# Kernel optimization log

Hardware: AMD Instinct MI355X
Metric: run time of the kernel (lower is better)

## Reference

```python
import jax, jax.numpy as jnp
import numpy as np

N_ATOMS = 8192
N_FINGERPRINT = 10000
DIM = 64
N_LAYERS = 3
N_MOL = 256


def setup_inputs() -> dict:
    key = jax.random.key(0)
    k1, k2, k3, k4, k5 = jax.random.split(key, 5)
    fingerprints = jax.random.randint(k1, (N_ATOMS,), 0, N_FINGERPRINT)
    adjacencies = jax.random.uniform(k2, (N_ATOMS, N_ATOMS), dtype=jnp.float32)
    segment_ids = jnp.sort(jax.random.randint(k3, (N_ATOMS,), 0, N_MOL))
    embed_table = jax.random.normal(k4, (N_FINGERPRINT, DIM), dtype=jnp.float32) * 0.1
    W = jax.random.normal(k5, (N_LAYERS, DIM, DIM), dtype=jnp.float32) * (1.0 / np.sqrt(DIM))
    b = jnp.zeros((N_LAYERS, DIM), dtype=jnp.float32)
    return {"fingerprints": fingerprints, "adjacencies": adjacencies,
            "segment_ids": segment_ids, "embed_table": embed_table, "W": W, "b": b}


def reference(fingerprints, adjacencies, segment_ids, embed_table, W, b):
    # Embed fingerprint indices -> [N_atoms, dim]
    vectors = embed_table[fingerprints]
    # MPNN layers: h = relu(Linear(v)); v = h + A @ h  (residual message passing)
    for layer in range(N_LAYERS):
        h = jax.nn.relu(jnp.einsum('nd,ed->ne', vectors, W[layer]) + b[layer])
        vectors = h + adjacencies @ h
    # Sum pooling per molecule (torch.split + sum == segment_sum over sorted ids)
    molecular_vectors = jax.ops.segment_sum(vectors, segment_ids, num_segments=N_MOL)
    return molecular_vectors
```

## Files before the change

kernel.cpp:

```cpp
#include <hip/hip_runtime.h>

#define N_ATOMS 8192
#define DIM 64
#define N_MOL 256
#define KS 16
#define KCH (N_ATOMS / KS)
#define BM 64
#define BN 64
#define BK 64
#define NSTEP (KCH / BK)

typedef __attribute__((ext_vector_type(8))) short short8v;
typedef __attribute__((ext_vector_type(4))) float f32x4;
typedef unsigned short ushort_t;

__device__ __forceinline__ ushort_t f2bf(float x) {
    unsigned u = __float_as_uint(x);
    u += 0x7fffu + ((u >> 16) & 1u);
    return (ushort_t)(u >> 16);
}

__device__ __forceinline__ void gload16(const void* gsrc, void* ldst) {
    __builtin_amdgcn_global_load_lds(
        (const __attribute__((address_space(1))) void*)gsrc,
        (__attribute__((address_space(3))) void*)ldst, 16, 0, 0);
}

__device__ __forceinline__ int lower_bound_dev(const int* __restrict__ seg, int val) {
    int lo = 0, hi = N_ATOMS;
    while (lo < hi) {
        int mid = (lo + hi) >> 1;
        if (seg[mid] < val) lo = mid + 1; else hi = mid;
    }
    return lo;
}

__global__ __launch_bounds__(256) void convert_kernel(
        const float* __restrict__ A, ushort_t* __restrict__ Abf) {
    const size_t total = (size_t)N_ATOMS * N_ATOMS;
    const size_t stride = (size_t)gridDim.x * 256 * 8;
    for (size_t i = ((size_t)blockIdx.x * 256 + threadIdx.x) * 8; i < total; i += stride) {
        float4 a0 = *(const float4*)(A + i);
        float4 a1 = *(const float4*)(A + i + 4);
        short8v vv;
        vv[0] = (short)f2bf(a0.x); vv[1] = (short)f2bf(a0.y);
        vv[2] = (short)f2bf(a0.z); vv[3] = (short)f2bf(a0.w);
        vv[4] = (short)f2bf(a1.x); vv[5] = (short)f2bf(a1.y);
        vv[6] = (short)f2bf(a1.z); vv[7] = (short)f2bf(a1.w);
        *(short8v*)(Abf + i) = vv;
    }
}

template <int FIRST>
__global__ __launch_bounds__(256) void fused_linear_kernel(
        const int* __restrict__ fp, const float* __restrict__ table,
        const float* __restrict__ vprev,
        const float* __restrict__ W, const float* __restrict__ b,
        float* __restrict__ vnext, ushort_t* __restrict__ hT) {
    __shared__ float Ws[DIM][DIM + 1];
    __shared__ float vsT[DIM][36];

    const int t = threadIdx.x;
    const int n0 = blockIdx.x * 32;
    for (int i = t; i < DIM * DIM; i += 256) Ws[i >> 6][i & 63] = W[i];
    for (int i = t; i < 32 * DIM; i += 256) {
        const int nl = i >> 6, d = i & 63;
        const size_t n = n0 + nl;
        float val;
        if (FIRST) val = table[(size_t)fp[n] * DIM + d];
        else       val = vprev[n * DIM + d];
        vsT[d][nl] = val;
    }
    __syncthreads();

    const int e = t & 63;
    const int g = t >> 6;
    float acc[8];
    const float be = b[e];
#pragma unroll
    for (int i = 0; i < 8; ++i) acc[i] = be;

    for (int d = 0; d < DIM; ++d) {
        const float w = Ws[e][d];
        const float4* vp = (const float4*)&vsT[d][g * 8];
        float4 x0 = vp[0], x1 = vp[1];
        acc[0] += w * x0.x; acc[1] += w * x0.y; acc[2] += w * x0.z; acc[3] += w * x0.w;
        acc[4] += w * x1.x; acc[5] += w * x1.y; acc[6] += w * x1.z; acc[7] += w * x1.w;
    }

    ushort_t hb[8];
#pragma unroll
    for (int i = 0; i < 8; ++i) {
        float hv = acc[i] > 0.f ? acc[i] : 0.f;
        vnext[(size_t)(n0 + g * 8 + i) * DIM + e] = hv;
        hb[i] = f2bf(hv);
    }
    *(short8v*)(hT + (size_t)e * N_ATOMS + n0 + g * 8) = *(short8v*)&hb[0];
}

__global__ __launch_bounds__(256) void matmul_mfma_kernel(
        const ushort_t* __restrict__ Abf, const ushort_t* __restrict__ hT,
        float* __restrict__ vnext) {
    __shared__ ushort_t Asw[2][BM * BK];
    __shared__ ushort_t Bsw[2][BN * BK];

    const int t  = threadIdx.x;
    const int w  = t >> 6;
    const int l  = t & 63;
    const int lm = l & 15;
    const int lq = l >> 4;
    const int r0 = blockIdx.x * BM;
    const size_t kc0 = (size_t)blockIdx.y * KCH;

    auto stage = [&](int bi, size_t kb) {
#pragma unroll
        for (int q = 0; q < 2; ++q) {
            const int i = q * 256 + t;
            const int r = i >> 3, s = i & 7;
            gload16(Abf + (size_t)(r0 + r) * N_ATOMS + kb + ((s ^ (r & 7)) << 3),
                    &Asw[bi][(q * 256 + w * 64) * 8]);
        }
#pragma unroll
        for (int q = 0; q < 2; ++q) {
            const int i = q * 256 + t;
            const int r = i >> 3, s = i & 7;
            gload16(hT + (size_t)r * N_ATOMS + kb + ((s ^ (r & 7)) << 3),
                    &Bsw[bi][(q * 256 + w * 64) * 8]);
        }
    };

    f32x4 acc[4];
#pragma unroll
    for (int n = 0; n < 4; ++n) acc[n] = (f32x4){0.f, 0.f, 0.f, 0.f};

    stage(0, kc0);

    for (int ks = 0; ks < NSTEP; ++ks) {
        const int bi = ks & 1;
        if (ks + 1 < NSTEP) {
            stage(bi ^ 1, kc0 + (size_t)(ks + 1) * BK);
            asm volatile("s_waitcnt vmcnt(4)" ::: "memory");
        } else {
            asm volatile("s_waitcnt vmcnt(0)" ::: "memory");
        }
        __builtin_amdgcn_s_barrier();
        asm volatile("" ::: "memory");
#pragma unroll
        for (int kki = 0; kki < 2; ++kki) {
            const int sx = ((kki * 4 + lq) ^ (lm & 7)) << 3;
            const int ra = w * 16 + lm;
            short8v a0 = *(const short8v*)&Asw[bi][ra * BK + sx];
            short8v b0 = *(const short8v*)&Bsw[bi][(lm)      * BK + sx];
            short8v b1 = *(const short8v*)&Bsw[bi][(lm + 16) * BK + sx];
            short8v b2 = *(const short8v*)&Bsw[bi][(lm + 32) * BK + sx];
            short8v b3 = *(const short8v*)&Bsw[bi][(lm + 48) * BK + sx];
            acc[0] = __builtin_amdgcn_mfma_f32_16x16x32_bf16(a0, b0, acc[0], 0, 0, 0);
            acc[1] = __builtin_amdgcn_mfma_f32_16x16x32_bf16(a0, b1, acc[1], 0, 0, 0);
            acc[2] = __builtin_amdgcn_mfma_f32_16x16x32_bf16(a0, b2, acc[2], 0, 0, 0);
            acc[3] = __builtin_amdgcn_mfma_f32_16x16x32_bf16(a0, b3, acc[3], 0, 0, 0);
        }
        asm volatile("" ::: "memory");
        __builtin_amdgcn_s_barrier();
        asm volatile("" ::: "memory");
    }

    const int rb = r0 + w * 16 + lq * 4;
#pragma unroll
    for (int j = 0; j < 4; ++j) {
        float* vp = vnext + (size_t)(rb + j) * DIM + lm;
#pragma unroll
        for (int n = 0; n < 4; ++n) atomicAdd(vp + n * 16, acc[n][j]);
    }
}

__global__ __launch_bounds__(256) void segsum_kernel(
        const float* __restrict__ v, const int* __restrict__ seg,
        float* __restrict__ out) {
    __shared__ float sm[4][DIM];
    const int m = blockIdx.x;
    const int d = threadIdx.x & 63;
    const int g = threadIdx.x >> 6;
    const int lo = lower_bound_dev(seg, m);
    const int hi = lower_bound_dev(seg, m + 1);
    float acc = 0.f;
    for (int n = lo + g; n < hi; n += 4) acc += v[(size_t)n * DIM + d];
    sm[g][d] = acc;
    __syncthreads();
    if (g == 0) out[(size_t)m * DIM + d] = sm[0][d] + sm[1][d] + sm[2][d] + sm[3][d];
}

extern "C" void kernel_launch(void* const* d_in, const int* in_sizes, int n_in,
                              void* d_out, int out_size, void* d_ws, size_t ws_size,
                              hipStream_t stream) {
    const int*   fp    = (const int*)d_in[0];
    const float* A     = (const float*)d_in[1];
    const int*   seg   = (const int*)d_in[2];
    const float* table = (const float*)d_in[3];
    const float* W     = (const float*)d_in[4];
    const float* b     = (const float*)d_in[5];
    float* out = (float*)d_out;

    float*    vA  = (float*)d_ws;
    float*    vB  = vA + (size_t)N_ATOMS * DIM;
    ushort_t* hT  = (ushort_t*)(vB + (size_t)N_ATOMS * DIM);
    ushort_t* Abf = hT + (size_t)DIM * N_ATOMS;

    dim3 mmgrid(N_ATOMS / BM, KS);

    convert_kernel<<<2048, 256, 0, stream>>>(A, Abf);
    fused_linear_kernel<1><<<N_ATOMS / 32, 256, 0, stream>>>(
        fp, table, nullptr, W, b, vA, hT);
    matmul_mfma_kernel<<<mmgrid, 256, 0, stream>>>(Abf, hT, vA);
    fused_linear_kernel<0><<<N_ATOMS / 32, 256, 0, stream>>>(
        fp, table, vA, W + DIM * DIM, b + DIM, vB, hT);
    matmul_mfma_kernel<<<mmgrid, 256, 0, stream>>>(Abf, hT, vB);
    fused_linear_kernel<0><<<N_ATOMS / 32, 256, 0, stream>>>(
        fp, table, vB, W + 2 * DIM * DIM, b + 2 * DIM, vA, hT);
    matmul_mfma_kernel<<<mmgrid, 256, 0, stream>>>(Abf, hT, vA);
    segsum_kernel<<<N_MOL, 256, 0, stream>>>(vA, seg, out);
}
```

Measured before the change: 226.5 us.

## Quantize adjacency to FP8 and split h into hi/lo FP8 with scaling

The adjacency matrix is converted to FP8 instead of BF16, which halves its footprint and the traffic of the dominant matmul. Each layer's h is packed into two FP8 terms (high part plus residual) using a per-layer power-of-two scale found with an atomic max. The matmul then runs two FP8 MFMAs per tile. Risks are accuracy loss on the adjacency values, plus an extra pack kernel and a memset per call.

Result: slower. 273.2 us (+20.6%).

```diff
diff --git a/kernel.cpp b/kernel.cpp
--- a/kernel.cpp
+++ b/kernel.cpp
@@ -12,13 +12,7 @@
 
 typedef __attribute__((ext_vector_type(8))) short short8v;
 typedef __attribute__((ext_vector_type(4))) float f32x4;
-typedef unsigned short ushort_t;
-
-__device__ __forceinline__ ushort_t f2bf(float x) {
-    unsigned u = __float_as_uint(x);
-    u += 0x7fffu + ((u >> 16) & 1u);
-    return (ushort_t)(u >> 16);
-}
+typedef unsigned char u8;
 
 __device__ __forceinline__ void gload16(const void* gsrc, void* ldst) {
     __builtin_amdgcn_global_load_lds(
@@ -35,19 +29,26 @@
     return lo;
 }
 
+__device__ __forceinline__ float scale_from_raw(int bits) {
+    if (bits <= 0) return 1.0f;
+    int e = (bits >> 23) - 127 - 7;
+    if (e < 0) e = 0;
+    return __int_as_float((e + 127) << 23);
+}
+
 __global__ __launch_bounds__(256) void convert_kernel(
-        const float* __restrict__ A, ushort_t* __restrict__ Abf) {
+        const float* __restrict__ A, u8* __restrict__ A8) {
     const size_t total = (size_t)N_ATOMS * N_ATOMS;
     const size_t stride = (size_t)gridDim.x * 256 * 8;
     for (size_t i = ((size_t)blockIdx.x * 256 + threadIdx.x) * 8; i < total; i += stride) {
         float4 a0 = *(const float4*)(A + i);
         float4 a1 = *(const float4*)(A + i + 4);
-        short8v vv;
-        vv[0] = (short)f2bf(a0.x); vv[1] = (short)f2bf(a0.y);
-        vv[2] = (short)f2bf(a0.z); vv[3] = (short)f2bf(a0.w);
-        vv[4] = (short)f2bf(a1.x); vv[5] = (short)f2bf(a1.y);
-        vv[6] = (short)f2bf(a1.z); vv[7] = (short)f2bf(a1.w);
-        *(short8v*)(Abf + i) = vv;
+        int p = __builtin_amdgcn_cvt_pk_fp8_f32(a0.x, a0.y, 0, 0);
+        p     = __builtin_amdgcn_cvt_pk_fp8_f32(a0.z, a0.w, p, 1);
+        int q = __builtin_amdgcn_cvt_pk_fp8_f32(a1.x, a1.y, 0, 0);
+        q     = __builtin_amdgcn_cvt_pk_fp8_f32(a1.z, a1.w, q, 1);
+        int2 v; v.x = p; v.y = q;
+        *(int2*)(A8 + i) = v;
     }
 }
 
@@ -56,7 +57,7 @@
         const int* __restrict__ fp, const float* __restrict__ table,
         const float* __restrict__ vprev,
         const float* __restrict__ W, const float* __restrict__ b,
-        float* __restrict__ vnext, ushort_t* __restrict__ hT) {
+        float* __restrict__ vnext, int* __restrict__ scaleRaw, int lay) {
     __shared__ float Ws[DIM][DIM + 1];
     __shared__ float vsT[DIM][36];
 
@@ -88,21 +89,61 @@
         acc[4] += w * x1.x; acc[5] += w * x1.y; acc[6] += w * x1.z; acc[7] += w * x1.w;
     }
 
-    ushort_t hb[8];
+    float hmax = 0.f;
 #pragma unroll
     for (int i = 0; i < 8; ++i) {
         float hv = acc[i] > 0.f ? acc[i] : 0.f;
         vnext[(size_t)(n0 + g * 8 + i) * DIM + e] = hv;
-        hb[i] = f2bf(hv);
-    }
-    *(short8v*)(hT + (size_t)e * N_ATOMS + n0 + g * 8) = *(short8v*)&hb[0];
+        hmax = hv > hmax ? hv : hmax;
+    }
+    atomicMax(scaleRaw + lay, __float_as_int(hmax));
+}
+
+__global__ __launch_bounds__(256) void pack_kernel(
+        const float* __restrict__ h, const int* __restrict__ scaleRaw, int lay,
+        u8* __restrict__ hT8) {
+    const float invS = 1.0f / scale_from_raw(scaleRaw[lay]);
+    const int t = threadIdx.x;
+    const int e = t & 63;
+    const int g = t >> 6;
+    const int nb = blockIdx.x * 32 + g * 8;
+
+    float y[8];
+#pragma unroll
+    for (int i = 0; i < 8; ++i) y[i] = h[(size_t)(nb + i) * DIM + e] * invS;
+
+    int hp0 = __builtin_amdgcn_cvt_pk_fp8_f32(y[0], y[1], 0, 0);
+    hp0     = __builtin_amdgcn_cvt_pk_fp8_f32(y[2], y[3], hp0, 1);
+    int hp1 = __builtin_amdgcn_cvt_pk_fp8_f32(y[4], y[5], 0, 0);
+    hp1     = __builtin_amdgcn_cvt_pk_fp8_f32(y[6], y[7], hp1, 1);
+
+    float r[8];
+    r[0] = y[0] - __builtin_amdgcn_cvt_f32_fp8(hp0, 0);
+    r[1] = y[1] - __builtin_amdgcn_cvt_f32_fp8(hp0, 1);
+    r[2] = y[2] - __builtin_amdgcn_cvt_f32_fp8(hp0, 2);
+    r[3] = y[3] - __builtin_amdgcn_cvt_f32_fp8(hp0, 3);
+    r[4] = y[4] - __builtin_amdgcn_cvt_f32_fp8(hp1, 0);
+    r[5] = y[5] - __builtin_amdgcn_cvt_f32_fp8(hp1, 1);
+    r[6] = y[6] - __builtin_amdgcn_cvt_f32_fp8(hp1, 2);
+    r[7] = y[7] - __builtin_amdgcn_cvt_f32_fp8(hp1, 3);
+
+    int lp0 = __builtin_amdgcn_cvt_pk_fp8_f32(r[0], r[1], 0, 0);
+    lp0     = __builtin_amdgcn_cvt_pk_fp8_f32(r[2], r[3], lp0, 1);
+    int lp1 = __builtin_amdgcn_cvt_pk_fp8_f32(r[4], r[5], 0, 0);
+    lp1     = __builtin_amdgcn_cvt_pk_fp8_f32(r[6], r[7], lp1, 1);
+
+    int2 hv; hv.x = hp0; hv.y = hp1;
+    int2 lv; lv.x = lp0; lv.y = lp1;
+    *(int2*)(hT8 + (size_t)e * N_ATOMS + nb) = hv;
+    *(int2*)(hT8 + (size_t)DIM * N_ATOMS + (size_t)e * N_ATOMS + nb) = lv;
 }
 
 __global__ __launch_bounds__(256) void matmul_mfma_kernel(
-        const ushort_t* __restrict__ Abf, const ushort_t* __restrict__ hT,
-        float* __restrict__ vnext) {
-    __shared__ ushort_t Asw[2][BM * BK];
-    __shared__ ushort_t Bsw[2][BN * BK];
+        const u8* __restrict__ A8, const u8* __restrict__ hT8,
+        const int* __restrict__ scaleRaw, int lay, float* __restrict__ vnext) {
+    __shared__ __align__(16) u8 Asw[2][BM * BK];
+    __shared__ __align__(16) u8 Bhi[2][BN * BK];
+    __shared__ __align__(16) u8 Blo[2][BN * BK];
 
     const int t  = threadIdx.x;
     const int w  = t >> 6;
@@ -111,22 +152,17 @@
     const int lq = l >> 4;
     const int r0 = blockIdx.x * BM;
     const size_t kc0 = (size_t)blockIdx.y * KCH;
+    const u8* hlo = hT8 + (size_t)DIM * N_ATOMS;
 
     auto stage = [&](int bi, size_t kb) {
-#pragma unroll
-        for (int q = 0; q < 2; ++q) {
-            const int i = q * 256 + t;
-            const int r = i >> 3, s = i & 7;
-            gload16(Abf + (size_t)(r0 + r) * N_ATOMS + kb + ((s ^ (r & 7)) << 3),
-                    &Asw[bi][(q * 256 + w * 64) * 8]);
-        }
-#pragma unroll
-        for (int q = 0; q < 2; ++q) {
-            const int i = q * 256 + t;
-            const int r = i >> 3, s = i & 7;
-            gload16(hT + (size_t)r * N_ATOMS + kb + ((s ^ (r & 7)) << 3),
-                    &Bsw[bi][(q * 256 + w * 64) * 8]);
-        }
+        const int r = t >> 2, s = t & 3;
+        const int src_off = ((s ^ (r & 3)) << 4);
+        gload16(A8 + (size_t)(r0 + r) * N_ATOMS + kb + src_off,
+                &Asw[bi][(w * 64) * 16]);
+        gload16(hT8 + (size_t)r * N_ATOMS + kb + src_off,
+                &Bhi[bi][(w * 64) * 16]);
+        gload16(hlo + (size_t)r * N_ATOMS + kb + src_off,
+                &Blo[bi][(w * 64) * 16]);
     };
 
     f32x4 acc[4];
@@ -139,7 +175,7 @@
         const int bi = ks & 1;
         if (ks + 1 < NSTEP) {
             stage(bi ^ 1, kc0 + (size_t)(ks + 1) * BK);
-            asm volatile("s_waitcnt vmcnt(4)" ::: "memory");
+            asm volatile("s_waitcnt vmcnt(3)" ::: "memory");
         } else {
             asm volatile("s_waitcnt vmcnt(0)" ::: "memory");
         }
@@ -147,29 +183,32 @@
         asm volatile("" ::: "memory");
 #pragma unroll
         for (int kki = 0; kki < 2; ++kki) {
-            const int sx = ((kki * 4 + lq) ^ (lm & 7)) << 3;
+            const int klog = kki * 2 + (lq >> 1);
+            const int within = (lq & 1) * 8;
             const int ra = w * 16 + lm;
-            short8v a0 = *(const short8v*)&Asw[bi][ra * BK + sx];
-            short8v b0 = *(const short8v*)&Bsw[bi][(lm)      * BK + sx];
-            short8v b1 = *(const short8v*)&Bsw[bi][(lm + 16) * BK + sx];
-            short8v b2 = *(const short8v*)&Bsw[bi][(lm + 32) * BK + sx];
-            short8v b3 = *(const short8v*)&Bsw[bi][(lm + 48) * BK + sx];
-            acc[0] = __builtin_amdgcn_mfma_f32_16x16x32_bf16(a0, b0, acc[0], 0, 0, 0);
-            acc[1] = __builtin_amdgcn_mfma_f32_16x16x32_bf16(a0, b1, acc[1], 0, 0, 0);
-            acc[2] = __builtin_amdgcn_mfma_f32_16x16x32_bf16(a0, b2, acc[2], 0, 0, 0);
-            acc[3] = __builtin_amdgcn_mfma_f32_16x16x32_bf16(a0, b3, acc[3], 0, 0, 0);
+            const long a = *(const long*)&Asw[bi][ra * BK + ((klog ^ (ra & 3)) << 4) + within];
+#pragma unroll
+            for (int n = 0; n < 4; ++n) {
+                const int rb = n * 16 + lm;
+                const int off = rb * BK + ((klog ^ (rb & 3)) << 4) + within;
+                const long bh = *(const long*)&Bhi[bi][off];
+                const long bl = *(const long*)&Blo[bi][off];
+                acc[n] = __builtin_amdgcn_mfma_f32_16x16x32_fp8_fp8(a, bh, acc[n], 0, 0, 0);
+                acc[n] = __builtin_amdgcn_mfma_f32_16x16x32_fp8_fp8(a, bl, acc[n], 0, 0, 0);
+            }
         }
         asm volatile("" ::: "memory");
         __builtin_amdgcn_s_barrier();
         asm volatile("" ::: "memory");
     }
 
+    const float S = scale_from_raw(scaleRaw[lay]);
     const int rb = r0 + w * 16 + lq * 4;
 #pragma unroll
     for (int j = 0; j < 4; ++j) {
         float* vp = vnext + (size_t)(rb + j) * DIM + lm;
 #pragma unroll
-        for (int n = 0; n < 4; ++n) atomicAdd(vp + n * 16, acc[n][j]);
+        for (int n = 0; n < 4; ++n) atomicAdd(vp + n * 16, acc[n][j] * S);
     }
 }
 
@@ -200,22 +239,29 @@
     const float* b     = (const float*)d_in[5];
     float* out = (float*)d_out;
 
-    float*    vA  = (float*)d_ws;
-    float*    vB  = vA + (size_t)N_ATOMS * DIM;
-    ushort_t* hT  = (ushort_t*)(vB + (size_t)N_ATOMS * DIM);
-    ushort_t* Abf = hT + (size_t)DIM * N_ATOMS;
+    char* ws = (char*)d_ws;
+    float* vA       = (float*)ws;
+    float* vB       = (float*)(ws + (size_t)2 * 1024 * 1024);
+    u8*    hT8      = (u8*)   (ws + (size_t)4 * 1024 * 1024);
+    int*   scaleRaw = (int*)  (ws + (size_t)5 * 1024 * 1024);
+    u8*    A8       = (u8*)   (ws + (size_t)5 * 1024 * 1024 + 256);
+
+    (void)hipMemsetAsync(scaleRaw, 0, 4 * sizeof(int), stream);
+    convert_kernel<<<2048, 256, 0, stream>>>(A, A8);
 
     dim3 mmgrid(N_ATOMS / BM, KS);
 
-    convert_kernel<<<2048, 256, 0, stream>>>(A, Abf);
     fused_linear_kernel<1><<<N_ATOMS / 32, 256, 0, stream>>>(
-        fp, table, nullptr, W, b, vA, hT);
-    matmul_mfma_kernel<<<mmgrid, 256, 0, stream>>>(Abf, hT, vA);
+        fp, table, nullptr, W, b, vA, scaleRaw, 0);
+    pack_kernel<<<N_ATOMS / 32, 256, 0, stream>>>(vA, scaleRaw, 0, hT8);
+    matmul_mfma_kernel<<<mmgrid, 256, 0, stream>>>(A8, hT8, scaleRaw, 0, vA);
     fused_linear_kernel<0><<<N_ATOMS / 32, 256, 0, stream>>>(
-        fp, table, vA, W + DIM * DIM, b + DIM, vB, hT);
-    matmul_mfma_kernel<<<mmgrid, 256, 0, stream>>>(Abf, hT, vB);
+        fp, table, vA, W + DIM * DIM, b + DIM, vB, scaleRaw, 1);
+    pack_kernel<<<N_ATOMS / 32, 256, 0, stream>>>(vB, scaleRaw, 1, hT8);
+    matmul_mfma_kernel<<<mmgrid, 256, 0, stream>>>(A8, hT8, scaleRaw, 1, vB);
     fused_linear_kernel<0><<<N_ATOMS / 32, 256, 0, stream>>>(
-        fp, table, vB, W + 2 * DIM * DIM, b + 2 * DIM, vA, hT);
-    matmul_mfma_kernel<<<mmgrid, 256, 0, stream>>>(Abf, hT, vA);
+        fp, table, vB, W + 2 * DIM * DIM, b + 2 * DIM, vA, scaleRaw, 2);
+    pack_kernel<<<N_ATOMS / 32, 256, 0, stream>>>(vA, scaleRaw, 2, hT8);
+    matmul_mfma_kernel<<<mmgrid, 256, 0, stream>>>(A8, hT8, scaleRaw, 2, vA);
     segsum_kernel<<<N_MOL, 256, 0, stream>>>(vA, seg, out);
 }
```

## Fold segment-sum into last layer via precomputed segment-summed adjacency

Applied to the files above, without the earlier changes.

Uses linearity: segsum(h + A h) = segsum(h) + (S·A) h. The conversion pass now also builds S·A (256×8192) with atomics while it converts A to bf16. The last 8192-row matmul is replaced by a 256-row matmul against the packed S·A, and the last linear layer accumulates segsum(h) straight into the output. This removes most of the third adjacency matmul and the separate segsum kernel, at the cost of extra atomics, two memsets and a 256×8192 workspace. S·A is rounded to bf16 from sums of many entries, which may add precision error.

New measurement: 218.7 us. -3.4%, faster.

```diff
diff --git a/kernel.cpp b/kernel.cpp
--- a/kernel.cpp
+++ b/kernel.cpp
@@ -26,42 +26,68 @@
         (__attribute__((address_space(3))) void*)ldst, 16, 0, 0);
 }
 
-__device__ __forceinline__ int lower_bound_dev(const int* __restrict__ seg, int val) {
-    int lo = 0, hi = N_ATOMS;
-    while (lo < hi) {
-        int mid = (lo + hi) >> 1;
-        if (seg[mid] < val) lo = mid + 1; else hi = mid;
-    }
-    return lo;
-}
-
-__global__ __launch_bounds__(256) void convert_kernel(
-        const float* __restrict__ A, ushort_t* __restrict__ Abf) {
-    const size_t total = (size_t)N_ATOMS * N_ATOMS;
-    const size_t stride = (size_t)gridDim.x * 256 * 8;
-    for (size_t i = ((size_t)blockIdx.x * 256 + threadIdx.x) * 8; i < total; i += stride) {
-        float4 a0 = *(const float4*)(A + i);
-        float4 a1 = *(const float4*)(A + i + 4);
-        short8v vv;
-        vv[0] = (short)f2bf(a0.x); vv[1] = (short)f2bf(a0.y);
-        vv[2] = (short)f2bf(a0.z); vv[3] = (short)f2bf(a0.w);
-        vv[4] = (short)f2bf(a1.x); vv[5] = (short)f2bf(a1.y);
-        vv[6] = (short)f2bf(a1.z); vv[7] = (short)f2bf(a1.w);
-        *(short8v*)(Abf + i) = vv;
-    }
-}
-
-template <int FIRST>
+__global__ __launch_bounds__(256) void convsa_kernel(
+        const float* __restrict__ A, const int* __restrict__ seg,
+        ushort_t* __restrict__ Abf, float* __restrict__ SAf32) {
+    const int t = threadIdx.x;
+    const int k = blockIdx.x * 512 + t * 2;
+    const int n0 = blockIdx.y * 128;
+    __shared__ int segs[128];
+    if (t < 128) segs[t] = seg[n0 + t];
+    __syncthreads();
+
+    float a0 = 0.f, a1 = 0.f;
+    int prev = segs[0];
+    for (int ni = 0; ni < 128; ni += 4) {
+        float2 v0 = *(const float2*)(A + (size_t)(n0 + ni + 0) * N_ATOMS + k);
+        float2 v1 = *(const float2*)(A + (size_t)(n0 + ni + 1) * N_ATOMS + k);
+        float2 v2 = *(const float2*)(A + (size_t)(n0 + ni + 2) * N_ATOMS + k);
+        float2 v3 = *(const float2*)(A + (size_t)(n0 + ni + 3) * N_ATOMS + k);
+        float2 vs[4] = {v0, v1, v2, v3};
+#pragma unroll
+        for (int j = 0; j < 4; ++j) {
+            const int m = segs[ni + j];
+            if (m != prev) {
+                atomicAdd(&SAf32[(size_t)prev * N_ATOMS + k],     a0);
+                atomicAdd(&SAf32[(size_t)prev * N_ATOMS + k + 1], a1);
+                a0 = a1 = 0.f; prev = m;
+            }
+            ushort2 bv; bv.x = f2bf(vs[j].x); bv.y = f2bf(vs[j].y);
+            *(ushort2*)(Abf + (size_t)(n0 + ni + j) * N_ATOMS + k) = bv;
+            a0 += vs[j].x; a1 += vs[j].y;
+        }
+    }
+    atomicAdd(&SAf32[(size_t)prev * N_ATOMS + k],     a0);
+    atomicAdd(&SAf32[(size_t)prev * N_ATOMS + k + 1], a1);
+}
+
+__global__ __launch_bounds__(256) void packsa_kernel(
+        const float* __restrict__ SAf32, ushort_t* __restrict__ SAbf) {
+    const size_t i = ((size_t)blockIdx.x * 256 + threadIdx.x) * 8;
+    float4 x0 = *(const float4*)(SAf32 + i);
+    float4 x1 = *(const float4*)(SAf32 + i + 4);
+    short8v v;
+    v[0] = (short)f2bf(x0.x); v[1] = (short)f2bf(x0.y);
+    v[2] = (short)f2bf(x0.z); v[3] = (short)f2bf(x0.w);
+    v[4] = (short)f2bf(x1.x); v[5] = (short)f2bf(x1.y);
+    v[6] = (short)f2bf(x1.z); v[7] = (short)f2bf(x1.w);
+    *(short8v*)(SAbf + i) = v;
+}
+
+template <int FIRST, int LAST>
 __global__ __launch_bounds__(256) void fused_linear_kernel(
         const int* __restrict__ fp, const float* __restrict__ table,
-        const float* __restrict__ vprev,
+        const float* __restrict__ vprev, const int* __restrict__ seg,
         const float* __restrict__ W, const float* __restrict__ b,
-        float* __restrict__ vnext, ushort_t* __restrict__ hT) {
+        float* __restrict__ vnext, ushort_t* __restrict__ hT,
+        float* __restrict__ out) {
     __shared__ float Ws[DIM][DIM + 1];
     __shared__ float vsT[DIM][36];
+    __shared__ int segs[32];
 
     const int t = threadIdx.x;
     const int n0 = blockIdx.x * 32;
+    if (LAST && t < 32) segs[t] = seg[n0 + t];
     for (int i = t; i < DIM * DIM; i += 256) Ws[i >> 6][i & 63] = W[i];
     for (int i = t; i < 32 * DIM; i += 256) {
         const int nl = i >> 6, d = i & 63;
@@ -89,12 +115,24 @@
     }
 
     ushort_t hb[8];
+    float seg_acc = 0.f;
+    int prev = LAST ? segs[g * 8] : 0;
 #pragma unroll
     for (int i = 0; i < 8; ++i) {
         float hv = acc[i] > 0.f ? acc[i] : 0.f;
-        vnext[(size_t)(n0 + g * 8 + i) * DIM + e] = hv;
+        if (LAST) {
+            const int m = segs[g * 8 + i];
+            if (m != prev) {
+                atomicAdd(&out[(size_t)prev * DIM + e], seg_acc);
+                seg_acc = 0.f; prev = m;
+            }
+            seg_acc += hv;
+        } else {
+            vnext[(size_t)(n0 + g * 8 + i) * DIM + e] = hv;
+        }
         hb[i] = f2bf(hv);
     }
+    if (LAST) atomicAdd(&out[(size_t)prev * DIM + e], seg_acc);
     *(short8v*)(hT + (size_t)e * N_ATOMS + n0 + g * 8) = *(short8v*)&hb[0];
 }
 
@@ -173,22 +211,6 @@
     }
 }
 
-__global__ __launch_bounds__(256) void segsum_kernel(
-        const float* __restrict__ v, const int* __restrict__ seg,
-        float* __restrict__ out) {
-    __shared__ float sm[4][DIM];
-    const int m = blockIdx.x;
-    const int d = threadIdx.x & 63;
-    const int g = threadIdx.x >> 6;
-    const int lo = lower_bound_dev(seg, m);
-    const int hi = lower_bound_dev(seg, m + 1);
-    float acc = 0.f;
-    for (int n = lo + g; n < hi; n += 4) acc += v[(size_t)n * DIM + d];
-    sm[g][d] = acc;
-    __syncthreads();
-    if (g == 0) out[(size_t)m * DIM + d] = sm[0][d] + sm[1][d] + sm[2][d] + sm[3][d];
-}
-
 extern "C" void kernel_launch(void* const* d_in, const int* in_sizes, int n_in,
                               void* d_out, int out_size, void* d_ws, size_t ws_size,
                               hipStream_t stream) {
@@ -200,22 +222,29 @@
     const float* b     = (const float*)d_in[5];
     float* out = (float*)d_out;
 
-    float*    vA  = (float*)d_ws;
-    float*    vB  = vA + (size_t)N_ATOMS * DIM;
-    ushort_t* hT  = (ushort_t*)(vB + (size_t)N_ATOMS * DIM);
-    ushort_t* Abf = hT + (size_t)DIM * N_ATOMS;
+    char* ws = (char*)d_ws;
+    float*    vA    = (float*)    ws;
+    float*    vB    = (float*)   (ws + 2097152);
+    ushort_t* hT    = (ushort_t*)(ws + 4194304);
+    float*    SAf32 = (float*)   (ws + 5242880);
+    ushort_t* SAbf  = (ushort_t*)(ws + 13631488);
+    ushort_t* Abf   = (ushort_t*)(ws + 17825792);
+
+    (void)hipMemsetAsync(SAf32, 0, (size_t)N_MOL * N_ATOMS * 4, stream);
+    (void)hipMemsetAsync(out, 0, (size_t)out_size * 4, stream);
+
+    convsa_kernel<<<dim3(16, 64), 256, 0, stream>>>(A, seg, Abf, SAf32);
+    packsa_kernel<<<(N_MOL * N_ATOMS) / (256 * 8), 256, 0, stream>>>(SAf32, SAbf);
 
     dim3 mmgrid(N_ATOMS / BM, KS);
 
-    convert_kernel<<<2048, 256, 0, stream>>>(A, Abf);
-    fused_linear_kernel<1><<<N_ATOMS / 32, 256, 0, stream>>>(
-        fp, table, nullptr, W, b, vA, hT);
+    fused_linear_kernel<1, 0><<<N_ATOMS / 32, 256, 0, stream>>>(
+        fp, table, nullptr, seg, W, b, vA, hT, nullptr);
     matmul_mfma_kernel<<<mmgrid, 256, 0, stream>>>(Abf, hT, vA);
-    fused_linear_kernel<0><<<N_ATOMS / 32, 256, 0, stream>>>(
-        fp, table, vA, W + DIM * DIM, b + DIM, vB, hT);
+    fused_linear_kernel<0, 0><<<N_ATOMS / 32, 256, 0, stream>>>(
+        fp, table, vA, seg, W + DIM * DIM, b + DIM, vB, hT, nullptr);
     matmul_mfma_kernel<<<mmgrid, 256, 0, stream>>>(Abf, hT, vB);
-    fused_linear_kernel<0><<<N_ATOMS / 32, 256, 0, stream>>>(
-        fp, table, vB, W + 2 * DIM * DIM, b + 2 * DIM, vA, hT);
-    matmul_mfma_kernel<<<mmgrid, 256, 0, stream>>>(Abf, hT, vA);
-    segsum_kernel<<<N_MOL, 256, 0, stream>>>(vA, seg, out);
-}
+    fused_linear_kernel<0, 1><<<N_ATOMS / 32, 256, 0, stream>>>(
+        fp, table, vB, seg, W + 2 * DIM * DIM, b + 2 * DIM, nullptr, hT, out);
+    matmul_mfma_kernel<<<dim3(N_MOL / BM, KS), 256, 0, stream>>>(SAbf, hT, out);
+}
```
